# Kernel optimization log

Hardware: AMD Instinct MI355X
Metric: run time of the kernel (lower is better)

Reference implementation:

```python
import jax, jax.numpy as jnp
import numpy as np

D_MODEL, H, D_K = 768, 12, 64
B, S = 2, 2048
NEG = -1.0e9


def setup_inputs() -> dict:
    key = jax.random.key(0)
    ks = jax.random.split(key, 7)
    q = jax.random.normal(ks[0], (B, S, D_MODEL), dtype=jnp.float32)
    k = jax.random.normal(ks[1], (B, S, D_MODEL), dtype=jnp.float32)
    v = jax.random.normal(ks[2], (B, S, D_MODEL), dtype=jnp.float32)
    mask = jnp.tril(jnp.ones((S, S), dtype=jnp.int32))[None, None]  # [1,1,S,S] causal
    sc = 1.0 / np.sqrt(D_MODEL)
    w_q = jax.random.normal(ks[3], (D_MODEL, D_MODEL), dtype=jnp.float32) * sc
    w_k = jax.random.normal(ks[4], (D_MODEL, D_MODEL), dtype=jnp.float32) * sc
    w_v = jax.random.normal(ks[5], (D_MODEL, D_MODEL), dtype=jnp.float32) * sc
    w_o = jax.random.normal(ks[6], (D_MODEL, D_MODEL), dtype=jnp.float32) * sc
    return {"q": q, "k": k, "v": v, "mask": mask,
            "w_q": w_q, "w_k": w_k, "w_v": w_v, "w_o": w_o}


def reference(q, k, v, mask, w_q, w_k, w_v, w_o):
    # nn.Linear(x) = x @ W.T ; split heads: [B,S,D] -> [B,H,S,Dk]
    def split_heads(x, w):
        y = jnp.einsum('bsd,ed->bse', x, w)
        return y.reshape(x.shape[0], x.shape[1], H, D_K).transpose(0, 2, 1, 3)

    qh = split_heads(q, w_q)
    kh = split_heads(k, w_k)
    vh = split_heads(v, w_v)
    scores = jnp.einsum('bhqd,bhkd->bhqk', qh, kh) / jnp.sqrt(jnp.float32(D_K))
    scores = jnp.where(mask == 0, jnp.float32(NEG), scores)
    attn = jax.nn.softmax(scores, axis=-1)  # dropout p=0 -> identity
    ctx = jnp.einsum('bhqk,bhkd->bhqd', attn, vh)
    ctx = ctx.transpose(0, 2, 1, 3).reshape(q.shape[0], q.shape[1], D_MODEL)
    return jnp.einsum('bsd,ed->bse', ctx, w_o)
```

## Files before the change

kernel.cpp:

```cpp
#include <hip/hip_runtime.h>

#define DM   768
#define HN   12
#define DKH  64
#define BSZ  2
#define SEQ  2048
#define MROWS (BSZ*SEQ)
#define NEGBIG -1.0e9f
#define NSLOT 40

typedef __bf16 bf16;
typedef __bf16 bf16x8 __attribute__((ext_vector_type(8)));
typedef __bf16 bf16x4 __attribute__((ext_vector_type(4)));
typedef float  f32x4  __attribute__((ext_vector_type(4)));
typedef unsigned int uint32;

__device__ __forceinline__ void gload_lds16(const void* g, void* l) {
    __builtin_amdgcn_global_load_lds(
        (const __attribute__((address_space(1))) char*)g,
        (__attribute__((address_space(3))) char*)l, 16, 0, 0);
}

__global__ __launch_bounds__(256) void cvt3(const float* __restrict__ a, const float* __restrict__ b,
                                            const float* __restrict__ c,
                                            bf16* __restrict__ x, bf16* __restrict__ y,
                                            bf16* __restrict__ z, int n) {
    const float* s; bf16* d;
    if      (blockIdx.y == 0) { s = a; d = x; }
    else if (blockIdx.y == 1) { s = b; d = y; }
    else                      { s = c; d = z; }
    int i = (blockIdx.x * 256 + threadIdx.x) * 4;
    if (i + 3 < n) {
        float4 v = *(const float4*)(s + i);
        bf16x4 o; o[0] = (bf16)v.x; o[1] = (bf16)v.y; o[2] = (bf16)v.z; o[3] = (bf16)v.w;
        *(bf16x4*)(d + i) = o;
    }
}
__global__ __launch_bounds__(256) void cvt4(const float* __restrict__ a, const float* __restrict__ b,
                                            const float* __restrict__ c, const float* __restrict__ e,
                                            bf16* __restrict__ x, bf16* __restrict__ y,
                                            bf16* __restrict__ z, bf16* __restrict__ u, int n) {
    const float* s; bf16* d;
    if      (blockIdx.y == 0) { s = a; d = x; }
    else if (blockIdx.y == 1) { s = b; d = y; }
    else if (blockIdx.y == 2) { s = c; d = z; }
    else                      { s = e; d = u; }
    int i = (blockIdx.x * 256 + threadIdx.x) * 4;
    if (i + 3 < n) {
        float4 v = *(const float4*)(s + i);
        bf16x4 o; o[0] = (bf16)v.x; o[1] = (bf16)v.y; o[2] = (bf16)v.z; o[3] = (bf16)v.w;
        *(bf16x4*)(d + i) = o;
    }
}

__global__ __launch_bounds__(256) void gemm_qkv(
    const bf16* __restrict__ xq, const bf16* __restrict__ xk, const bf16* __restrict__ xv,
    const bf16* __restrict__ wq, const bf16* __restrict__ wk, const bf16* __restrict__ wv,
    bf16* __restrict__ qh, bf16* __restrict__ kh, bf16* __restrict__ vt)
{
    __shared__ bf16 As[128 * 32];
    __shared__ bf16 Bs[128 * 32];

    const bf16* A; const bf16* Bw; bf16* Out;
    if      (blockIdx.z == 0) { A = xq; Bw = wq; Out = qh; }
    else if (blockIdx.z == 1) { A = xk; Bw = wk; Out = kh; }
    else                      { A = xv; Bw = wv; Out = vt; }
    const bool vout = (blockIdx.z == 2);

    const int t = threadIdx.x, w = t >> 6, lane = t & 63;
    const int mt = blockIdx.x * 128, nt = blockIdx.y * 128;
    const int wr = (w >> 1) * 64, wc = (w & 1) * 64;

    f32x4 acc[4][4] = {};

    for (int k0 = 0; k0 < DM; k0 += 32) {
        #pragma unroll
        for (int i = 0; i < 2; i++) {
            int c = i * 256 + t;
            int row = c >> 2, col = (c & 3) * 8;
            gload_lds16(A  + (size_t)(mt + row) * DM + k0 + col, (char*)As + c * 16);
            gload_lds16(Bw + (size_t)(nt + row) * DM + k0 + col, (char*)Bs + c * 16);
        }
        asm volatile("s_waitcnt vmcnt(0)" ::: "memory");
        __syncthreads();

        bf16x8 af[4], bfr[4];
        #pragma unroll
        for (int m = 0; m < 4; m++)
            af[m] = *(const bf16x8*)&As[(wr + m * 16 + (lane & 15)) * 32 + (lane >> 4) * 8];
        #pragma unroll
        for (int n = 0; n < 4; n++)
            bfr[n] = *(const bf16x8*)&Bs[(wc + n * 16 + (lane & 15)) * 32 + (lane >> 4) * 8];
        #pragma unroll
        for (int m = 0; m < 4; m++)
            #pragma unroll
            for (int n = 0; n < 4; n++)
                acc[m][n] = __builtin_amdgcn_mfma_f32_16x16x32_bf16(af[m], bfr[n], acc[m][n], 0, 0, 0);
        __syncthreads();
    }

    if (!vout) {
        #pragma unroll
        for (int m = 0; m < 4; m++) {
            #pragma unroll
            for (int n = 0; n < 4; n++) {
                #pragma unroll
                for (int r = 0; r < 4; r++) {
                    int gm = mt + wr + m * 16 + (lane >> 4) * 4 + r;
                    int gn = nt + wc + n * 16 + (lane & 15);
                    int b = gm >> 11, s = gm & 2047, h = gn >> 6, d = gn & 63;
                    Out[(((size_t)b * HN + h) * SEQ + s) * DKH + d] = (bf16)acc[m][n][r];
                }
            }
        }
    } else {
        #pragma unroll
        for (int m = 0; m < 4; m++) {
            #pragma unroll
            for (int n = 0; n < 4; n++) {
                int gm = mt + wr + m * 16 + (lane >> 4) * 4;
                int gn = nt + wc + n * 16 + (lane & 15);
                int b = gm >> 11, s0 = gm & 2047, h = gn >> 6, d = gn & 63;
                bf16x4 pk;
                #pragma unroll
                for (int r = 0; r < 4; r++) pk[r] = (bf16)acc[m][n][r];
                *(bf16x4*)&Out[(((size_t)b * HN + h) * DKH + d) * SEQ + s0] = pk;
            }
        }
    }
}

__global__ __launch_bounds__(256) void gemm_out(
    const bf16* __restrict__ Actx, const bf16* __restrict__ Bw, float* __restrict__ Out)
{
    __shared__ bf16 As[128 * 32];
    __shared__ bf16 Bs[128 * 32];

    const int t = threadIdx.x, w = t >> 6, lane = t & 63;
    const int mt = blockIdx.x * 128, nt = blockIdx.y * 128;
    const int wr = (w >> 1) * 64, wc = (w & 1) * 64;

    f32x4 acc[4][4] = {};

    for (int k0 = 0; k0 < DM; k0 += 32) {
        #pragma unroll
        for (int i = 0; i < 2; i++) {
            int c = i * 256 + t;
            int row = c >> 2, col = (c & 3) * 8;
            gload_lds16(Actx + (size_t)(mt + row) * DM + k0 + col, (char*)As + c * 16);
            gload_lds16(Bw   + (size_t)(nt + row) * DM + k0 + col, (char*)Bs + c * 16);
        }
        asm volatile("s_waitcnt vmcnt(0)" ::: "memory");
        __syncthreads();

        bf16x8 af[4], bfr[4];
        #pragma unroll
        for (int m = 0; m < 4; m++)
            af[m] = *(const bf16x8*)&As[(wr + m * 16 + (lane & 15)) * 32 + (lane >> 4) * 8];
        #pragma unroll
        for (int n = 0; n < 4; n++)
            bfr[n] = *(const bf16x8*)&Bs[(wc + n * 16 + (lane & 15)) * 32 + (lane >> 4) * 8];
        #pragma unroll
        for (int m = 0; m < 4; m++)
            #pragma unroll
            for (int n = 0; n < 4; n++)
                acc[m][n] = __builtin_amdgcn_mfma_f32_16x16x32_bf16(af[m], bfr[n], acc[m][n], 0, 0, 0);
        __syncthreads();
    }

    #pragma unroll
    for (int m = 0; m < 4; m++) {
        #pragma unroll
        for (int n = 0; n < 4; n++) {
            #pragma unroll
            for (int r = 0; r < 4; r++) {
                int gm = mt + wr + m * 16 + (lane >> 4) * 4 + r;
                int gn = nt + wc + n * 16 + (lane & 15);
                Out[(size_t)gm * DM + gn] = acc[m][n][r];
            }
        }
    }
}

__global__ __launch_bounds__(256, 3) void flash_split(
    const bf16* __restrict__ qh, const bf16* __restrict__ kh,
    const bf16* __restrict__ vt, bf16* __restrict__ ctx,
    bf16* __restrict__ pO, float* __restrict__ pM, float* __restrict__ pL)
{
    __shared__ bf16 Ks[2][4096];
    __shared__ bf16 Vs[2][4096];
    __shared__ bf16 pl[4][32 * 72];

    const int bid = blockIdx.x;
    const int slot = bid / 24;
    const int bh = bid % 24;

    int qt, p, np;
    if (slot < 16)      { qt = 15 - (slot >> 2); p = slot & 3;  np = 4; }
    else if (slot < 28) { int s = slot - 16; qt = 11 - s / 3; p = s % 3; np = 3; }
    else if (slot < 36) { int s = slot - 28; qt = 7 - (s >> 1); p = s & 1; np = 2; }
    else                { qt = 39 - slot; p = 0; np = 1; }

    const int T = 2 * qt + 2;
    const int bse = T / np, rem = T - bse * np;
    const int cnt   = bse + (p < rem ? 1 : 0);
    const int start = p * bse + (p < rem ? p : rem);

    const int qb = qt * 128;
    const int t = threadIdx.x, w = t >> 6, lane = t & 63;
    const int g = lane >> 4, lo = lane & 15;
    const size_t base = (size_t)bh * SEQ * DKH;
    const char* khead = (const char*)(kh + base);
    const char* vhead = (const char*)(vt + base);

    uint32 koff[2], voff[2];
    #pragma unroll
    for (int i = 0; i < 2; i++) {
        int c = w * 128 + i * 64 + lane;
        int r = c >> 3, s = c & 7;
        int sw = s ^ (r & 7);
        koff[i] = (uint32)(r * 128  + 16 * sw);
        voff[i] = (uint32)(r * 4096 + 16 * sw);
    }
    const uint32 kr0 = (uint32)(128 * lo + 16 * (g ^ (lo & 7)));
    const uint32 kr1 = kr0 ^ 64;

    const int qrow0 = qb + 16 * w + lo;
    const int qrow1 = qb + 64 + 16 * w + lo;
    const bf16* qp0 = qh + base + (size_t)qrow0 * DKH + g * 8;
    const bf16* qp1 = qh + base + (size_t)qrow1 * DKH + g * 8;
    bf16x8 qa0 = *(const bf16x8*)qp0;
    bf16x8 qa1 = *(const bf16x8*)(qp0 + 32);
    bf16x8 qb0 = *(const bf16x8*)qp1;
    bf16x8 qb1 = *(const bf16x8*)(qp1 + 32);

    f32x4 O0[4] = {}, O1[4] = {};
    float m0 = -1e30f, l0 = 0.0f, m1 = -1e30f, l1 = 0.0f;
    bf16* plw = &pl[w][0];

    #pragma unroll
    for (int i = 0; i < 2; i++) {
        int c16 = (w * 128 + i * 64 + lane) * 16;
        gload_lds16(khead + (size_t)start * 8192 + koff[i], (char*)&Ks[0][0] + c16);
        gload_lds16(vhead + (size_t)start * 128  + voff[i], (char*)&Vs[0][0] + c16);
    }
    asm volatile("s_waitcnt vmcnt(0)" ::: "memory");
    __syncthreads();

    for (int it = 0; it < cnt; ++it) {
        const int kt = start + it;
        const int par = it & 1, nxt = par ^ 1;
        if (it + 1 < cnt) {
            const char* ks = khead + (size_t)(kt + 1) * 8192;
            const char* vs = vhead + (size_t)(kt + 1) * 128;
            #pragma unroll
            for (int i = 0; i < 2; i++) {
                int c16 = (w * 128 + i * 64 + lane) * 16;
                gload_lds16(ks + koff[i], (char*)&Ks[nxt][0] + c16);
                gload_lds16(vs + voff[i], (char*)&Vs[nxt][0] + c16);
            }
        }

        const bool act0  = (kt != T - 1);
        const bool diag0 = (kt == T - 2);
        const bool diag1 = (kt == T - 1);

        const char* Kp = (const char*)&Ks[par][0];
        f32x4 s0[4], s1[4];
        {
            bf16x8 kf0[4], kf1[4];
            #pragma unroll
            for (int cg = 0; cg < 4; cg++) {
                kf0[cg] = *(const bf16x8*)(Kp + cg * 2048 + kr0);
                kf1[cg] = *(const bf16x8*)(Kp + cg * 2048 + kr1);
            }
            __builtin_amdgcn_s_setprio(1);
            if (act0) {
                #pragma unroll
                for (int cg = 0; cg < 4; cg++) {
                    f32x4 z = {0.0f, 0.0f, 0.0f, 0.0f};
                    z = __builtin_amdgcn_mfma_f32_16x16x32_bf16(kf0[cg], qa0, z, 0, 0, 0);
                    z = __builtin_amdgcn_mfma_f32_16x16x32_bf16(kf1[cg], qa1, z, 0, 0, 0);
                    s0[cg] = z;
                }
            }
            #pragma unroll
            for (int cg = 0; cg < 4; cg++) {
                f32x4 z = {0.0f, 0.0f, 0.0f, 0.0f};
                z = __builtin_amdgcn_mfma_f32_16x16x32_bf16(kf0[cg], qb0, z, 0, 0, 0);
                z = __builtin_amdgcn_mfma_f32_16x16x32_bf16(kf1[cg], qb1, z, 0, 0, 0);
                s1[cg] = z;
            }
            __builtin_amdgcn_s_setprio(0);
        }

        if (act0) {
            if (diag0) {
                #pragma unroll
                for (int cg = 0; cg < 4; cg++)
                    #pragma unroll
                    for (int r = 0; r < 4; r++) {
                        int ki = kt * 64 + cg * 16 + 4 * g + r;
                        float v = s0[cg][r] * 0.125f;
                        s0[cg][r] = (ki > qrow0) ? NEGBIG : v;
                    }
            } else {
                #pragma unroll
                for (int cg = 0; cg < 4; cg++)
                    #pragma unroll
                    for (int r = 0; r < 4; r++) s0[cg][r] *= 0.125f;
            }
        }
        if (diag1) {
            #pragma unroll
            for (int cg = 0; cg < 4; cg++)
                #pragma unroll
                for (int r = 0; r < 4; r++) {
                    int ki = kt * 64 + cg * 16 + 4 * g + r;
                    float v = s1[cg][r] * 0.125f;
                    s1[cg][r] = (ki > qrow1) ? NEGBIG : v;
                }
        } else {
            #pragma unroll
            for (int cg = 0; cg < 4; cg++)
                #pragma unroll
                for (int r = 0; r < 4; r++) s1[cg][r] *= 0.125f;
        }

        if (act0) {
            float mx = fmaxf(fmaxf(fmaxf(s0[0][0], s0[0][1]), fmaxf(s0[0][2], s0[0][3])),
                             fmaxf(fmaxf(s0[1][0], s0[1][1]), fmaxf(s0[1][2], s0[1][3])));
            mx = fmaxf(mx, fmaxf(fmaxf(fmaxf(s0[2][0], s0[2][1]), fmaxf(s0[2][2], s0[2][3])),
                                 fmaxf(fmaxf(s0[3][0], s0[3][1]), fmaxf(s0[3][2], s0[3][3]))));
            mx = fmaxf(mx, __shfl_xor(mx, 16, 64));
            mx = fmaxf(mx, __shfl_xor(mx, 32, 64));
            if (!__all(mx - m0 <= 8.0f)) {
                float mnew = fmaxf(m0, mx);
                float scl = __expf(m0 - mnew);
                m0 = mnew; l0 *= scl;
                float s4[4];
                #pragma unroll
                for (int r = 0; r < 4; r++) s4[r] = __shfl(scl, 4 * g + r, 64);
                #pragma unroll
                for (int dg = 0; dg < 4; dg++)
                    #pragma unroll
                    for (int r = 0; r < 4; r++) O0[dg][r] *= s4[r];
            }
            float rs = 0.0f;
            #pragma unroll
            for (int cg = 0; cg < 4; cg++)
                #pragma unroll
                for (int r = 0; r < 4; r++) {
                    s0[cg][r] = __expf(s0[cg][r] - m0);
                    rs += s0[cg][r];
                }
            rs += __shfl_xor(rs, 16, 64);
            rs += __shfl_xor(rs, 32, 64);
            l0 += rs;
            #pragma unroll
            for (int cg = 0; cg < 4; cg++) {
                bf16x4 pk;
                #pragma unroll
                for (int r = 0; r < 4; r++) pk[r] = (bf16)s0[cg][r];
                *(bf16x4*)&plw[lo * 72 + cg * 16 + 4 * g] = pk;
            }
        }
        {
            float mx = fmaxf(fmaxf(fmaxf(s1[0][0], s1[0][1]), fmaxf(s1[0][2], s1[0][3])),
                             fmaxf(fmaxf(s1[1][0], s1[1][1]), fmaxf(s1[1][2], s1[1][3])));
            mx = fmaxf(mx, fmaxf(fmaxf(fmaxf(s1[2][0], s1[2][1]), fmaxf(s1[2][2], s1[2][3])),
                                 fmaxf(fmaxf(s1[3][0], s1[3][1]), fmaxf(s1[3][2], s1[3][3]))));
            mx = fmaxf(mx, __shfl_xor(mx, 16, 64));
            mx = fmaxf(mx, __shfl_xor(mx, 32, 64));
            if (!__all(mx - m1 <= 8.0f)) {
                float mnew = fmaxf(m1, mx);
                float scl = __expf(m1 - mnew);
                m1 = mnew; l1 *= scl;
                float s4[4];
                #pragma unroll
                for (int r = 0; r < 4; r++) s4[r] = __shfl(scl, 4 * g + r, 64);
                #pragma unroll
                for (int dg = 0; dg < 4; dg++)
                    #pragma unroll
                    for (int r = 0; r < 4; r++) O1[dg][r] *= s4[r];
            }
            float rs = 0.0f;
            #pragma unroll
            for (int cg = 0; cg < 4; cg++)
                #pragma unroll
                for (int r = 0; r < 4; r++) {
                    s1[cg][r] = __expf(s1[cg][r] - m1);
                    rs += s1[cg][r];
                }
            rs += __shfl_xor(rs, 16, 64);
            rs += __shfl_xor(rs, 32, 64);
            l1 += rs;
            #pragma unroll
            for (int cg = 0; cg < 4; cg++) {
                bf16x4 pk;
                #pragma unroll
                for (int r = 0; r < 4; r++) pk[r] = (bf16)s1[cg][r];
                *(bf16x4*)&plw[(16 + lo) * 72 + cg * 16 + 4 * g] = pk;
            }
        }

        {
            const char* Vp = (const char*)&Vs[par][0];
            bf16x8 vv[8];
            #pragma unroll
            for (int kq = 0; kq < 2; kq++)
                #pragma unroll
                for (int dblk = 0; dblk < 4; dblk++)
                    vv[kq * 4 + dblk] = *(const bf16x8*)
                        (Vp + (dblk * 16 + lo) * 128 + 16 * ((4 * kq + g) ^ (lo & 7)));
            __builtin_amdgcn_s_setprio(1);
            if (act0) {
                #pragma unroll
                for (int kq = 0; kq < 2; kq++) {
                    bf16x8 pa = *(const bf16x8*)&plw[lo * 72 + kq * 32 + 8 * g];
                    #pragma unroll
                    for (int dblk = 0; dblk < 4; dblk++)
                        O0[dblk] = __builtin_amdgcn_mfma_f32_16x16x32_bf16(pa, vv[kq * 4 + dblk], O0[dblk], 0, 0, 0);
                }
            }
            #pragma unroll
            for (int kq = 0; kq < 2; kq++) {
                bf16x8 pa = *(const bf16x8*)&plw[(16 + lo) * 72 + kq * 32 + 8 * g];
                #pragma unroll
                for (int dblk = 0; dblk < 4; dblk++)
                    O1[dblk] = __builtin_amdgcn_mfma_f32_16x16x32_bf16(pa, vv[kq * 4 + dblk], O1[dblk], 0, 0, 0);
            }
            __builtin_amdgcn_s_setprio(0);
        }

        asm volatile("s_waitcnt vmcnt(0)" ::: "memory");
        __syncthreads();
    }

    if (np == 1) {
        const int b = bh / HN, h = bh % HN;
        float inv0[4], inv1[4];
        #pragma unroll
        for (int r = 0; r < 4; r++) {
            inv0[r] = 1.0f / __shfl(l0, 4 * g + r, 64);
            inv1[r] = 1.0f / __shfl(l1, 4 * g + r, 64);
        }
        #pragma unroll
        for (int dg = 0; dg < 4; dg++) {
            #pragma unroll
            for (int r = 0; r < 4; r++) {
                int row0 = qb + 16 * w + g * 4 + r;
                int row1 = qb + 64 + 16 * w + g * 4 + r;
                ctx[((size_t)(b * SEQ + row0)) * DM + h * DKH + dg * 16 + lo] =
                    (bf16)(O0[dg][r] * inv0[r]);
                ctx[((size_t)(b * SEQ + row1)) * DM + h * DKH + dg * 16 + lo] =
                    (bf16)(O1[dg][r] * inv1[r]);
            }
        }
    } else {
        const int pslot = bh * NSLOT + slot;
        bf16* po = pO + (size_t)pslot * 128 * 64;
        #pragma unroll
        for (int dg = 0; dg < 4; dg++) {
            #pragma unroll
            for (int r = 0; r < 4; r++) {
                int r0 = 16 * w + 4 * g + r;
                po[r0 * 64 + dg * 16 + lo]        = (bf16)O0[dg][r];
                po[(64 + r0) * 64 + dg * 16 + lo] = (bf16)O1[dg][r];
            }
        }
        if (g == 0) {
            pM[pslot * 128 + 16 * w + lo]      = m0;
            pL[pslot * 128 + 16 * w + lo]      = l0;
            pM[pslot * 128 + 64 + 16 * w + lo] = m1;
            pL[pslot * 128 + 64 + 16 * w + lo] = l1;
        }
    }
}

__global__ __launch_bounds__(256) void flash_combine(
    const bf16* __restrict__ pO, const float* __restrict__ pM,
    const float* __restrict__ pL, bf16* __restrict__ ctx)
{
    const int bh = blockIdx.x;
    const int qt = 4 + blockIdx.y;
    int np, s0;
    if (qt >= 12)     { np = 4; s0 = (15 - qt) * 4; }
    else if (qt >= 8) { np = 3; s0 = 16 + (11 - qt) * 3; }
    else              { np = 2; s0 = 28 + (7 - qt) * 2; }

    const int t = threadIdx.x;
    const int row = t >> 1, dh = (t & 1) * 32;
    const int pbase = bh * NSLOT + s0;

    float mi[4], wi[4];
    float mstar = -1e30f;
    #pragma unroll
    for (int i = 0; i < 4; i++)
        if (i < np) { mi[i] = pM[(pbase + i) * 128 + row]; mstar = fmaxf(mstar, mi[i]); }
    float lsum = 0.0f;
    #pragma unroll
    for (int i = 0; i < 4; i++)
        if (i < np) { wi[i] = __expf(mi[i] - mstar); lsum += wi[i] * pL[(pbase + i) * 128 + row]; }
    const float linv = 1.0f / lsum;

    const int b = bh / HN, h = bh % HN;
    bf16* crow = ctx + ((size_t)(b * SEQ + qt * 128 + row)) * DM + h * DKH + dh;

    #pragma unroll
    for (int d0 = 0; d0 < 32; d0 += 8) {
        float acc[8] = {};
        #pragma unroll
        for (int i = 0; i < 4; i++) {
            if (i < np) {
                bf16x8 o = *(const bf16x8*)&pO[((size_t)(pbase + i) * 128 + row) * 64 + dh + d0];
                #pragma unroll
                for (int j = 0; j < 8; j++) acc[j] += wi[i] * (float)o[j];
            }
        }
        bf16x8 ov;
        #pragma unroll
        for (int j = 0; j < 8; j++) ov[j] = (bf16)(acc[j] * linv);
        *(bf16x8*)(crow + d0) = ov;
    }
}

extern "C" void kernel_launch(void* const* d_in, const int* in_sizes, int n_in,
                              void* d_out, int out_size, void* d_ws, size_t ws_size,
                              hipStream_t stream) {
    const float* q  = (const float*)d_in[0];
    const float* k  = (const float*)d_in[1];
    const float* v  = (const float*)d_in[2];
    const float* wq = (const float*)d_in[4];
    const float* wk = (const float*)d_in[5];
    const float* wv = (const float*)d_in[6];
    const float* wo = (const float*)d_in[7];
    float* out = (float*)d_out;

    const size_t NX = (size_t)MROWS * DM;
    const size_t NW = (size_t)DM * DM;

    bf16* p = (bf16*)d_ws;
    bf16* xq  = p; p += NX;
    bf16* xk  = p; p += NX;
    bf16* xv  = p; p += NX;
    bf16* wqb = p; p += NW;
    bf16* wkb = p; p += NW;
    bf16* wvb = p; p += NW;
    bf16* wob = p; p += NW;
    bf16* qhp = p; p += NX;
    bf16* khp = p; p += NX;
    bf16* vtp = p; p += NX;
    bf16* ctxp = p; p += NX;

    bf16*  pO = xq;
    float* pM = (float*)(xq + (size_t)24 * NSLOT * 128 * 64);
    float* pL = pM + 24 * NSLOT * 128;

    cvt3<<<dim3(NX / 1024, 3), 256, 0, stream>>>(q, k, v, xq, xk, xv, (int)NX);
    cvt4<<<dim3(NW / 1024, 4), 256, 0, stream>>>(wq, wk, wv, wo, wqb, wkb, wvb, wob, (int)NW);

    gemm_qkv<<<dim3(MROWS / 128, DM / 128, 3), 256, 0, stream>>>(
        xq, xk, xv, wqb, wkb, wvb, qhp, khp, vtp);

    flash_split<<<24 * NSLOT, 256, 0, stream>>>(qhp, khp, vtp, ctxp, pO, pM, pL);
    flash_combine<<<dim3(24, 12), 256, 0, stream>>>(pO, pM, pL, ctxp);

    gemm_out<<<dim3(MROWS / 128, DM / 128), 256, 0, stream>>>(ctxp, wob, out);
}
```

Measured before the change: 105.7 us.

## Fuse fp32 input conversion into QKV GEMM, fold softmax scale into Q, shrink flash LDS

The QKV GEMM now loads fp32 activations straight into LDS through a swizzled layout and converts them to bf16 when building fragments, so the separate cvt3 conversion kernel and its bf16 round-trip through global memory are gone. The 1/sqrt(dk)*log2(e) factor is folded into the Q projection output, so the flash kernel can drop its per-score multiply and use exp2. The flash kernel's P staging buffer is halved and swizzled, with the two row groups sharing it in sequence, and occupancy is raised to 4 blocks per CU. The trade-offs are double-size A tiles in LDS and twice the global reads for the GEMM A operand, plus extra lgkm waits between the two P passes.

```diff
diff --git a/kernel.cpp b/kernel.cpp
--- a/kernel.cpp
+++ b/kernel.cpp
@@ -8,6 +8,7 @@
 #define MROWS (BSZ*SEQ)
 #define NEGBIG -1.0e9f
 #define NSLOT 40
+#define QSCALE 0.18033688011112042f
 
 typedef __bf16 bf16;
 typedef __bf16 bf16x8 __attribute__((ext_vector_type(8)));
@@ -21,21 +22,6 @@
         (__attribute__((address_space(3))) char*)l, 16, 0, 0);
 }
 
-__global__ __launch_bounds__(256) void cvt3(const float* __restrict__ a, const float* __restrict__ b,
-                                            const float* __restrict__ c,
-                                            bf16* __restrict__ x, bf16* __restrict__ y,
-                                            bf16* __restrict__ z, int n) {
-    const float* s; bf16* d;
-    if      (blockIdx.y == 0) { s = a; d = x; }
-    else if (blockIdx.y == 1) { s = b; d = y; }
-    else                      { s = c; d = z; }
-    int i = (blockIdx.x * 256 + threadIdx.x) * 4;
-    if (i + 3 < n) {
-        float4 v = *(const float4*)(s + i);
-        bf16x4 o; o[0] = (bf16)v.x; o[1] = (bf16)v.y; o[2] = (bf16)v.z; o[3] = (bf16)v.w;
-        *(bf16x4*)(d + i) = o;
-    }
-}
 __global__ __launch_bounds__(256) void cvt4(const float* __restrict__ a, const float* __restrict__ b,
                                             const float* __restrict__ c, const float* __restrict__ e,
                                             bf16* __restrict__ x, bf16* __restrict__ y,
@@ -54,31 +40,37 @@
 }
 
 __global__ __launch_bounds__(256) void gemm_qkv(
-    const bf16* __restrict__ xq, const bf16* __restrict__ xk, const bf16* __restrict__ xv,
+    const float* __restrict__ xq, const float* __restrict__ xk, const float* __restrict__ xv,
     const bf16* __restrict__ wq, const bf16* __restrict__ wk, const bf16* __restrict__ wv,
     bf16* __restrict__ qh, bf16* __restrict__ kh, bf16* __restrict__ vt)
 {
-    __shared__ bf16 As[128 * 32];
-    __shared__ bf16 Bs[128 * 32];
-
-    const bf16* A; const bf16* Bw; bf16* Out;
-    if      (blockIdx.z == 0) { A = xq; Bw = wq; Out = qh; }
-    else if (blockIdx.z == 1) { A = xk; Bw = wk; Out = kh; }
-    else                      { A = xv; Bw = wv; Out = vt; }
+    __shared__ float Asf[128 * 32];
+    __shared__ bf16  Bs[128 * 32];
+
+    const float* A; const bf16* Bw; bf16* Out; float qs;
+    if      (blockIdx.z == 0) { A = xq; Bw = wq; Out = qh; qs = QSCALE; }
+    else if (blockIdx.z == 1) { A = xk; Bw = wk; Out = kh; qs = 1.0f; }
+    else                      { A = xv; Bw = wv; Out = vt; qs = 1.0f; }
     const bool vout = (blockIdx.z == 2);
 
     const int t = threadIdx.x, w = t >> 6, lane = t & 63;
+    const int g = lane >> 4, lo = lane & 15;
     const int mt = blockIdx.x * 128, nt = blockIdx.y * 128;
     const int wr = (w >> 1) * 64, wc = (w & 1) * 64;
 
     f32x4 acc[4][4] = {};
 
     for (int k0 = 0; k0 < DM; k0 += 32) {
+        #pragma unroll
+        for (int i = 0; i < 4; i++) {
+            int c = i * 256 + t;
+            int row = c >> 3, cc = (c & 7) ^ (row & 7);
+            gload_lds16(A + (size_t)(mt + row) * DM + k0 + cc * 4, (char*)Asf + c * 16);
+        }
         #pragma unroll
         for (int i = 0; i < 2; i++) {
             int c = i * 256 + t;
             int row = c >> 2, col = (c & 3) * 8;
-            gload_lds16(A  + (size_t)(mt + row) * DM + k0 + col, (char*)As + c * 16);
             gload_lds16(Bw + (size_t)(nt + row) * DM + k0 + col, (char*)Bs + c * 16);
         }
         asm volatile("s_waitcnt vmcnt(0)" ::: "memory");
@@ -86,11 +78,19 @@
 
         bf16x8 af[4], bfr[4];
         #pragma unroll
-        for (int m = 0; m < 4; m++)
-            af[m] = *(const bf16x8*)&As[(wr + m * 16 + (lane & 15)) * 32 + (lane >> 4) * 8];
+        for (int m = 0; m < 4; m++) {
+            int row = wr + m * 16 + lo;
+            const char* rp = (const char*)Asf + row * 128;
+            float4 f0 = *(const float4*)(rp + (((2 * g)     ^ (lo & 7)) << 4));
+            float4 f1 = *(const float4*)(rp + (((2 * g + 1) ^ (lo & 7)) << 4));
+            bf16x8 a;
+            a[0] = (bf16)f0.x; a[1] = (bf16)f0.y; a[2] = (bf16)f0.z; a[3] = (bf16)f0.w;
+            a[4] = (bf16)f1.x; a[5] = (bf16)f1.y; a[6] = (bf16)f1.z; a[7] = (bf16)f1.w;
+            af[m] = a;
+        }
         #pragma unroll
         for (int n = 0; n < 4; n++)
-            bfr[n] = *(const bf16x8*)&Bs[(wc + n * 16 + (lane & 15)) * 32 + (lane >> 4) * 8];
+            bfr[n] = *(const bf16x8*)&Bs[(wc + n * 16 + lo) * 32 + g * 8];
         #pragma unroll
         for (int m = 0; m < 4; m++)
             #pragma unroll
@@ -106,10 +106,10 @@
             for (int n = 0; n < 4; n++) {
                 #pragma unroll
                 for (int r = 0; r < 4; r++) {
-                    int gm = mt + wr + m * 16 + (lane >> 4) * 4 + r;
-                    int gn = nt + wc + n * 16 + (lane & 15);
+                    int gm = mt + wr + m * 16 + g * 4 + r;
+                    int gn = nt + wc + n * 16 + lo;
                     int b = gm >> 11, s = gm & 2047, h = gn >> 6, d = gn & 63;
-                    Out[(((size_t)b * HN + h) * SEQ + s) * DKH + d] = (bf16)acc[m][n][r];
+                    Out[(((size_t)b * HN + h) * SEQ + s) * DKH + d] = (bf16)(acc[m][n][r] * qs);
                 }
             }
         }
@@ -118,8 +118,8 @@
         for (int m = 0; m < 4; m++) {
             #pragma unroll
             for (int n = 0; n < 4; n++) {
-                int gm = mt + wr + m * 16 + (lane >> 4) * 4;
-                int gn = nt + wc + n * 16 + (lane & 15);
+                int gm = mt + wr + m * 16 + g * 4;
+                int gn = nt + wc + n * 16 + lo;
                 int b = gm >> 11, s0 = gm & 2047, h = gn >> 6, d = gn & 63;
                 bf16x4 pk;
                 #pragma unroll
@@ -182,14 +182,14 @@
     }
 }
 
-__global__ __launch_bounds__(256, 3) void flash_split(
+__global__ __launch_bounds__(256, 4) void flash_split(
     const bf16* __restrict__ qh, const bf16* __restrict__ kh,
     const bf16* __restrict__ vt, bf16* __restrict__ ctx,
     bf16* __restrict__ pO, float* __restrict__ pM, float* __restrict__ pL)
 {
     __shared__ bf16 Ks[2][4096];
     __shared__ bf16 Vs[2][4096];
-    __shared__ bf16 pl[4][32 * 72];
+    __shared__ bf16 pl[4][1024];
 
     const int bid = blockIdx.x;
     const int slot = bid / 24;
@@ -224,6 +224,15 @@
     }
     const uint32 kr0 = (uint32)(128 * lo + 16 * (g ^ (lo & 7)));
     const uint32 kr1 = kr0 ^ 64;
+
+    uint32 pw[4], pr[2];
+    #pragma unroll
+    for (int cg = 0; cg < 4; cg++)
+        pw[cg] = (uint32)(lo * 128 + (((2 * cg + (g >> 1)) ^ (lo & 7)) << 4) + (g & 1) * 8);
+    #pragma unroll
+    for (int kq = 0; kq < 2; kq++)
+        pr[kq] = (uint32)(lo * 128 + (((4 * kq + g) ^ (lo & 7)) << 4));
+    char* plb = (char*)&pl[w][0];
 
     const int qrow0 = qb + 16 * w + lo;
     const int qrow1 = qb + 64 + 16 * w + lo;
@@ -236,7 +245,6 @@
 
     f32x4 O0[4] = {}, O1[4] = {};
     float m0 = -1e30f, l0 = 0.0f, m1 = -1e30f, l1 = 0.0f;
-    bf16* plw = &pl[w][0];
 
     #pragma unroll
     for (int i = 0; i < 2; i++) {
@@ -294,37 +302,23 @@
             __builtin_amdgcn_s_setprio(0);
         }
 
-        if (act0) {
-            if (diag0) {
-                #pragma unroll
-                for (int cg = 0; cg < 4; cg++)
-                    #pragma unroll
-                    for (int r = 0; r < 4; r++) {
-                        int ki = kt * 64 + cg * 16 + 4 * g + r;
-                        float v = s0[cg][r] * 0.125f;
-                        s0[cg][r] = (ki > qrow0) ? NEGBIG : v;
-                    }
-            } else {
-                #pragma unroll
-                for (int cg = 0; cg < 4; cg++)
-                    #pragma unroll
-                    for (int r = 0; r < 4; r++) s0[cg][r] *= 0.125f;
-            }
-        }
-        if (diag1) {
+        if (act0 && diag0) {
             #pragma unroll
             for (int cg = 0; cg < 4; cg++)
                 #pragma unroll
                 for (int r = 0; r < 4; r++) {
                     int ki = kt * 64 + cg * 16 + 4 * g + r;
-                    float v = s1[cg][r] * 0.125f;
-                    s1[cg][r] = (ki > qrow1) ? NEGBIG : v;
+                    s0[cg][r] = (ki > qrow0) ? NEGBIG : s0[cg][r];
                 }
-        } else {
+        }
+        if (diag1) {
             #pragma unroll
             for (int cg = 0; cg < 4; cg++)
                 #pragma unroll
-                for (int r = 0; r < 4; r++) s1[cg][r] *= 0.125f;
+                for (int r = 0; r < 4; r++) {
+                    int ki = kt * 64 + cg * 16 + 4 * g + r;
+                    s1[cg][r] = (ki > qrow1) ? NEGBIG : s1[cg][r];
+                }
         }
 
         if (act0) {
@@ -336,7 +330,7 @@
             mx = fmaxf(mx, __shfl_xor(mx, 32, 64));
             if (!__all(mx - m0 <= 8.0f)) {
                 float mnew = fmaxf(m0, mx);
-                float scl = __expf(m0 - mnew);
+                float scl = __builtin_exp2f(m0 - mnew);
                 m0 = mnew; l0 *= scl;
                 float s4[4];
                 #pragma unroll
@@ -351,19 +345,12 @@
             for (int cg = 0; cg < 4; cg++)
                 #pragma unroll
                 for (int r = 0; r < 4; r++) {
-                    s0[cg][r] = __expf(s0[cg][r] - m0);
+                    s0[cg][r] = __builtin_exp2f(s0[cg][r] - m0);
                     rs += s0[cg][r];
                 }
             rs += __shfl_xor(rs, 16, 64);
             rs += __shfl_xor(rs, 32, 64);
             l0 += rs;
-            #pragma unroll
-            for (int cg = 0; cg < 4; cg++) {
-                bf16x4 pk;
-                #pragma unroll
-                for (int r = 0; r < 4; r++) pk[r] = (bf16)s0[cg][r];
-                *(bf16x4*)&plw[lo * 72 + cg * 16 + 4 * g] = pk;
-            }
         }
         {
             float mx = fmaxf(fmaxf(fmaxf(s1[0][0], s1[0][1]), fmaxf(s1[0][2], s1[0][3])),
@@ -374,7 +361,7 @@
             mx = fmaxf(mx, __shfl_xor(mx, 32, 64));
             if (!__all(mx - m1 <= 8.0f)) {
                 float mnew = fmaxf(m1, mx);
-                float scl = __expf(m1 - mnew);
+                float scl = __builtin_exp2f(m1 - mnew);
                 m1 = mnew; l1 *= scl;
                 float s4[4];
                 #pragma unroll
@@ -389,43 +376,60 @@
             for (int cg = 0; cg < 4; cg++)
                 #pragma unroll
                 for (int r = 0; r < 4; r++) {
-                    s1[cg][r] = __expf(s1[cg][r] - m1);
+                    s1[cg][r] = __builtin_exp2f(s1[cg][r] - m1);
                     rs += s1[cg][r];
                 }
             rs += __shfl_xor(rs, 16, 64);
             rs += __shfl_xor(rs, 32, 64);
             l1 += rs;
+        }
+
+        const char* Vp = (const char*)&Vs[par][0];
+        bf16x8 vv[8];
+        #pragma unroll
+        for (int kq = 0; kq < 2; kq++)
+            #pragma unroll
+            for (int dblk = 0; dblk < 4; dblk++)
+                vv[kq * 4 + dblk] = *(const bf16x8*)
+                    (Vp + (dblk * 16 + lo) * 128 + 16 * ((4 * kq + g) ^ (lo & 7)));
+
+        if (act0) {
             #pragma unroll
             for (int cg = 0; cg < 4; cg++) {
                 bf16x4 pk;
                 #pragma unroll
+                for (int r = 0; r < 4; r++) pk[r] = (bf16)s0[cg][r];
+                *(bf16x4*)(plb + pw[cg]) = pk;
+            }
+        }
+        asm volatile("s_waitcnt lgkmcnt(0)" ::: "memory");
+        __builtin_amdgcn_sched_barrier(0);
+        if (act0) {
+            __builtin_amdgcn_s_setprio(1);
+            #pragma unroll
+            for (int kq = 0; kq < 2; kq++) {
+                bf16x8 pa = *(const bf16x8*)(plb + pr[kq]);
+                #pragma unroll
+                for (int dblk = 0; dblk < 4; dblk++)
+                    O0[dblk] = __builtin_amdgcn_mfma_f32_16x16x32_bf16(pa, vv[kq * 4 + dblk], O0[dblk], 0, 0, 0);
+            }
+            __builtin_amdgcn_s_setprio(0);
+        }
+        __builtin_amdgcn_sched_barrier(0);
+        {
+            #pragma unroll
+            for (int cg = 0; cg < 4; cg++) {
+                bf16x4 pk;
+                #pragma unroll
                 for (int r = 0; r < 4; r++) pk[r] = (bf16)s1[cg][r];
-                *(bf16x4*)&plw[(16 + lo) * 72 + cg * 16 + 4 * g] = pk;
-            }
-        }
-
-        {
-            const char* Vp = (const char*)&Vs[par][0];
-            bf16x8 vv[8];
-            #pragma unroll
-            for (int kq = 0; kq < 2; kq++)
-                #pragma unroll
-                for (int dblk = 0; dblk < 4; dblk++)
-                    vv[kq * 4 + dblk] = *(const bf16x8*)
-                        (Vp + (dblk * 16 + lo) * 128 + 16 * ((4 * kq + g) ^ (lo & 7)));
+                *(bf16x4*)(plb + pw[cg]) = pk;
+            }
+            asm volatile("s_waitcnt lgkmcnt(0)" ::: "memory");
+            __builtin_amdgcn_sched_barrier(0);
             __builtin_amdgcn_s_setprio(1);
-            if (act0) {
-                #pragma unroll
-                for (int kq = 0; kq < 2; kq++) {
-                    bf16x8 pa = *(const bf16x8*)&plw[lo * 72 + kq * 32 + 8 * g];
-                    #pragma unroll
-                    for (int dblk = 0; dblk < 4; dblk++)
-                        O0[dblk] = __builtin_amdgcn_mfma_f32_16x16x32_bf16(pa, vv[kq * 4 + dblk], O0[dblk], 0, 0, 0);
-                }
-            }
             #pragma unroll
             for (int kq = 0; kq < 2; kq++) {
-                bf16x8 pa = *(const bf16x8*)&plw[(16 + lo) * 72 + kq * 32 + 8 * g];
+                bf16x8 pa = *(const bf16x8*)(plb + pr[kq]);
                 #pragma unroll
                 for (int dblk = 0; dblk < 4; dblk++)
                     O1[dblk] = __builtin_amdgcn_mfma_f32_16x16x32_bf16(pa, vv[kq * 4 + dblk], O1[dblk], 0, 0, 0);
@@ -501,7 +505,7 @@
     float lsum = 0.0f;
     #pragma unroll
     for (int i = 0; i < 4; i++)
-        if (i < np) { wi[i] = __expf(mi[i] - mstar); lsum += wi[i] * pL[(pbase + i) * 128 + row]; }
+        if (i < np) { wi[i] = __builtin_exp2f(mi[i] - mstar); lsum += wi[i] * pL[(pbase + i) * 128 + row]; }
     const float linv = 1.0f / lsum;
 
     const int b = bh / HN, h = bh % HN;
@@ -541,9 +545,6 @@
     const size_t NW = (size_t)DM * DM;
 
     bf16* p = (bf16*)d_ws;
-    bf16* xq  = p; p += NX;
-    bf16* xk  = p; p += NX;
-    bf16* xv  = p; p += NX;
     bf16* wqb = p; p += NW;
     bf16* wkb = p; p += NW;
     bf16* wvb = p; p += NW;
@@ -552,16 +553,14 @@
     bf16* khp = p; p += NX;
     bf16* vtp = p; p += NX;
     bf16* ctxp = p; p += NX;
-
-    bf16*  pO = xq;
-    float* pM = (float*)(xq + (size_t)24 * NSLOT * 128 * 64);
+    bf16* pO = p; p += (size_t)24 * NSLOT * 128 * 64;
+    float* pM = (float*)p;
     float* pL = pM + 24 * NSLOT * 128;
 
-    cvt3<<<dim3(NX / 1024, 3), 256, 0, stream>>>(q, k, v, xq, xk, xv, (int)NX);
     cvt4<<<dim3(NW / 1024, 4), 256, 0, stream>>>(wq, wk, wv, wo, wqb, wkb, wvb, wob, (int)NW);
 
     gemm_qkv<<<dim3(MROWS / 128, DM / 128, 3), 256, 0, stream>>>(
-        xq, xk, xv, wqb, wkb, wvb, qhp, khp, vtp);
+        q, k, v, wqb, wkb, wvb, qhp, khp, vtp);
 
     flash_split<<<24 * NSLOT, 256, 0, stream>>>(qhp, khp, vtp, ctxp, pO, pM, pL);
     flash_combine<<<dim3(24, 12), 256, 0, stream>>>(pO, pM, pL, ctxp);
```

Measured after the change: 118.5 us. 1.12x slower.
